# Kernel tuning notes

Hardware: AMD Instinct MI355X
Metric: run time of the kernel (lower is better)

Reference implementation:

```python
import jax, jax.numpy as jnp
import numpy as np

ALPHA = 4.0  # surrogate.Sigmoid(alpha=4.0)
V_TH = 0.1
V_RESET = 0.0

@jax.custom_vjp
def spike(x):
    # Heaviside forward (spikingjelly surrogate.Sigmoid forward pass)
    return (x >= 0).astype(x.dtype)

def _spike_fwd(x):
    return spike(x), x

def _spike_bwd(x, g):
    sig = jax.nn.sigmoid(ALPHA * x)
    return (g * ALPHA * sig * (1.0 - sig),)

spike.defvjp(_spike_fwd, _spike_bwd)

def lif_multistep(x_seq, tau):
    # MultiStepPmLIFNode, hard reset, v clamped to [-2, 2]
    tau = jnp.clip(tau, 0.5, 5.0)
    inv_tau = 1.0 / tau
    def step(v, x):
        v = v + inv_tau * (-(v - V_RESET) + x)
        s = spike(v - V_TH)
        v = jnp.clip(v * (1.0 - s) + V_RESET * s, -2.0, 2.0)
        return v, s
    v0 = jnp.zeros_like(x_seq[0])
    _, spikes = jax.lax.scan(step, v0, x_seq)
    return spikes

def time_distributed_conv(x_seq, W, b, pad):
    # x_seq: [T, B, C, H, W]
    T, B, C, H, Wd = x_seq.shape
    x = x_seq.reshape(T * B, C, H, Wd)
    y = jax.lax.conv_general_dilated(
        x, W, window_strides=(1, 1), padding=[(pad, pad), (pad, pad)],
        dimension_numbers=('NCHW', 'OIHW', 'NCHW'))
    y = y + b[None, :, None, None]
    return y.reshape(T, B, W.shape[0], H, Wd)

def setup_inputs() -> dict:
    key = jax.random.key(0)
    ks = jax.random.split(key, 4)
    B, H, Wd = 8, 128, 128
    return {
        'lr_lab': jax.random.normal(ks[0], (B, 3, H, Wd), dtype=jnp.float32),
        'W1': jax.random.normal(ks[1], (64, 3, 3, 3), dtype=jnp.float32) * 0.1,
        'b1': jnp.zeros((64,), dtype=jnp.float32),
        'tau1': jnp.asarray(2.0, dtype=jnp.float32),
        'W2': jax.random.normal(ks[2], (64, 64, 3, 3), dtype=jnp.float32) * 0.05,
        'b2': jnp.zeros((64,), dtype=jnp.float32),
        'tau2': jnp.asarray(2.0, dtype=jnp.float32),
        'Wh': jax.random.normal(ks[3], (3, 64, 1, 1), dtype=jnp.float32) * 0.1,
        'bh': jnp.zeros((3,), dtype=jnp.float32),
        'T': 5,
    }

def reference(lr_lab, W1, b1, tau1, W2, b2, tau2, Wh, bh, T):
    # H=W=128 is already a power of 2, so the reflect-pad branch is a no-op.
    # TemporalEncoder('repeat') -> [T, B, C, H, W]
    lab_seq = jnp.broadcast_to(lr_lab[None], (T,) + lr_lab.shape)
    # init_conv1: Conv2d(3, 64, 3, pad=1) + MultiStepPmLIFNode
    feat = lif_multistep(time_distributed_conv(lab_seq, W1, b1, pad=1), tau1)
    # init_conv2: Conv2d(64, 64, 3, pad=1) + MultiStepPmLIFNode
    feat = lif_multistep(time_distributed_conv(feat, W2, b2, pad=1), tau2)
    # head_conv: Conv2d(64, 3, 1)
    feat_3 = time_distributed_conv(feat, Wh, bh, pad=0)
    return feat_3
```

## Files before the change

kernel.cpp:

```cpp
#include <hip/hip_runtime.h>


#define NB    8
#define HW    128
#define NPIX  (HW*HW)
#define NT    5

__global__ void k_transpose_w2(const float* __restrict__ W2, float* __restrict__ Wt) {
    int i = blockIdx.x * 256 + threadIdx.x;
    if (i >= 9 * 64 * 64) return;
    int oc = i & 63;
    int ic = (i >> 6) & 63;
    int tap = i >> 12;
    Wt[i] = W2[(oc * 64 + ic) * 9 + tap];
}

__global__ __launch_bounds__(256) void k_conv1_lif1(
    const float* __restrict__ lab, const float* __restrict__ W1,
    const float* __restrict__ b1, const float* __restrict__ tau1,
    unsigned long long* __restrict__ smask)
{
#pragma clang fp contract(off)
    __shared__ float w1s[64 * 27];
    __shared__ float b1s[64];
    {
        int tid = threadIdx.x;
        for (int e = tid; e < 64 * 27; e += 256) w1s[e] = W1[e];
        if (tid < 64) b1s[tid] = b1[tid];
        __syncthreads();
    }
    int g = blockIdx.x * 256 + threadIdx.x;
    int oc = g & 63;
    int x = (g >> 6) & (HW - 1);
    int y = (g >> 13) & (HW - 1);
    int b = g >> 20;

    const float* wbase = w1s + oc * 27;
    const float* ibase = lab + b * 3 * NPIX;
    float acc = 0.f;
    for (int kh = 0; kh < 3; ++kh) {
        int yy = y + kh - 1;
        if ((unsigned)yy >= (unsigned)HW) continue;
        for (int kw = 0; kw < 3; ++kw) {
            int xx = x + kw - 1;
            if ((unsigned)xx >= (unsigned)HW) continue;
            const float* px = ibase + yy * HW + xx;
#pragma unroll
            for (int ic = 0; ic < 3; ++ic) {
                acc = __builtin_fmaf(wbase[ic * 9 + kh * 3 + kw], px[ic * NPIX], acc);
            }
        }
    }
    float xin = acc + b1s[oc];

    float tauc = fminf(fmaxf(tau1[0], 0.5f), 5.0f);
    float it = 1.0f / tauc;

    float v = 0.f;
    unsigned bits = 0;
    for (int t = 0; t < NT; ++t) {
        float d = xin - v;
        float m = it * d;
        v = v + m;
        bool s = (v - 0.1f) >= 0.f;
        float vr = s ? 0.f : v;
        vr = fmaxf(vr, -2.f);
        vr = fminf(vr, 2.f);
        v = vr;
        if (s) bits |= (1u << t);
    }
    for (int t = 0; t < NT; ++t) {
        unsigned long long bal = __ballot((bits >> t) & 1);
        if (oc == 0) smask[((size_t)(b * NT + t) * NPIX) + y * HW + x] = bal;
    }
}

#define SEG(IC0, IC1, M, SH, PN)                                        \
    for (int ic = IC0; ic < IC1; ++ic) {                                \
        unsigned wb = wtu[ic * 64];                                     \
        _Pragma("unroll")                                               \
        for (int p = 0; p < 8; ++p) {                                   \
            unsigned sel = wb & (unsigned)(-(int)((M[p] >> (ic - SH)) & 1u)); \
            acc[p][PN] = acc[p][PN] + __uint_as_float(sel);             \
        }                                                               \
    }

#define TAP(KH, KW, SEGS) {                                             \
    const int yy = y + KH - 1;                                          \
    const bool vy = (unsigned)yy < (unsigned)HW;                        \
    unsigned Mlo[8], Mhi[8];                                            \
    _Pragma("unroll")                                                   \
    for (int p = 0; p < 8; ++p) {                                       \
        int xx = x0 + KW - 1 + p;                                       \
        unsigned long long mm = (vy && (unsigned)xx < (unsigned)HW)     \
                                ? smb[yy * HW + xx] : 0ULL;             \
        Mlo[p] = (unsigned)mm; Mhi[p] = (unsigned)(mm >> 32);           \
    }                                                                   \
    const unsigned* wtu = (const unsigned*)(Wt + (KH * 3 + KW) * 4096) + oc; \
    SEGS }

__global__ __launch_bounds__(256) void k_conv2_lif2(
    const unsigned long long* __restrict__ smask,
    const float* __restrict__ Wt, const float* __restrict__ b2,
    const float* __restrict__ tau2, unsigned long long* __restrict__ s2m)
{
#pragma clang fp contract(off)
    const int tid = threadIdx.x;
    const int oc = tid & 63;
    const int wid = __builtin_amdgcn_readfirstlane(blockIdx.x * 4 + (tid >> 6));
    const int b = wid >> 11;
    const int rem = wid & 2047;
    const int y = rem >> 4;
    const int x0 = (rem & 15) * 8;

    const float b2oc = b2[oc];
    float tauc = fminf(fmaxf(tau2[0], 0.5f), 5.0f);
    const float it = 1.0f / tauc;

    float v[8];
    for (int t = 0; t < NT; ++t) {
        float acc[8][4];
#pragma unroll
        for (int p = 0; p < 8; ++p) {
            acc[p][0] = 0.f; acc[p][1] = 0.f; acc[p][2] = 0.f; acc[p][3] = 0.f;
        }
        const unsigned long long* smb = smask + (size_t)(b * NT + t) * NPIX;

        TAP(0, 0, SEG(0,32,Mlo,0,0)  SEG(32,64,Mhi,32,0))
        TAP(0, 1, SEG(0,32,Mlo,0,0)  SEG(32,64,Mhi,32,0))
        TAP(0, 2, SEG(0,24,Mlo,0,0)  SEG(24,32,Mlo,0,1)  SEG(32,64,Mhi,32,1))
        TAP(1, 0, SEG(0,32,Mlo,0,1)  SEG(32,64,Mhi,32,1))
        TAP(1, 1, SEG(0,32,Mlo,0,1)  SEG(32,48,Mhi,32,1) SEG(48,64,Mhi,32,2))
        TAP(1, 2, SEG(0,32,Mlo,0,2)  SEG(32,64,Mhi,32,2))
        TAP(2, 0, SEG(0,32,Mlo,0,2)  SEG(32,64,Mhi,32,2))
        TAP(2, 1, SEG(0,8,Mlo,0,2)   SEG(8,32,Mlo,0,3)   SEG(32,64,Mhi,32,3))
        TAP(2, 2, SEG(0,32,Mlo,0,3)  SEG(32,64,Mhi,32,3))

        unsigned long long* s2mb = s2m + (size_t)(b * NT + t) * NPIX;
#pragma unroll
        for (int p = 0; p < 8; ++p) {
            float x2 = (((acc[p][0] + acc[p][1]) + acc[p][2]) + acc[p][3]) + b2oc;
            float vp = (t == 0) ? 0.f : v[p];
            float d = x2 - vp;
            float m = it * d;
            vp = vp + m;
            bool s = (vp - 0.1f) >= 0.f;
            float vr = s ? 0.f : vp;
            vr = fmaxf(vr, -2.f);
            vr = fminf(vr, 2.f);
            v[p] = vr;
            unsigned long long bal = __ballot(s);
            if (oc == 0) s2mb[y * HW + x0 + p] = bal;
        }
    }
}

__global__ __launch_bounds__(256) void k_head(
    const unsigned long long* __restrict__ s2m, const float* __restrict__ Wh,
    const float* __restrict__ bh, float* __restrict__ out)
{
#pragma clang fp contract(off)
    __shared__ float whs[192];
    __shared__ float bhs[3];
    {
        int tid = threadIdx.x;
        if (tid < 192) whs[tid] = Wh[tid];
        if (tid < 3) bhs[tid] = bh[tid];
        __syncthreads();
    }
    int g = blockIdx.x * 256 + threadIdx.x;
    int px = g & (NPIX - 1);
    int r = g >> 14;
    int b = r & 7;
    int t = r >> 3;

    unsigned long long m = s2m[(size_t)(b * NT + t) * NPIX + px];
    unsigned mlo = (unsigned)m, mhi = (unsigned)(m >> 32);
    float c0 = 0.f, c1 = 0.f, c2 = 0.f;
    for (int oc = 0; oc < 32; ++oc) {
        unsigned bit = (mlo >> oc) & 1u;
        if (bit) { c0 = c0 + whs[oc]; c1 = c1 + whs[64 + oc]; c2 = c2 + whs[128 + oc]; }
    }
    for (int oc = 32; oc < 64; ++oc) {
        unsigned bit = (mhi >> (oc - 32)) & 1u;
        if (bit) { c0 = c0 + whs[oc]; c1 = c1 + whs[64 + oc]; c2 = c2 + whs[128 + oc]; }
    }
    int obase = ((t * NB + b) * 3) * NPIX + px;
    out[obase] = c0 + bhs[0];
    out[obase + NPIX] = c1 + bhs[1];
    out[obase + 2 * NPIX] = c2 + bhs[2];
}

extern "C" void kernel_launch(void* const* d_in, const int* in_sizes, int n_in,
                              void* d_out, int out_size, void* d_ws, size_t ws_size,
                              hipStream_t stream) {
    const float* lab  = (const float*)d_in[0];
    const float* W1   = (const float*)d_in[1];
    const float* b1   = (const float*)d_in[2];
    const float* tau1 = (const float*)d_in[3];
    const float* W2   = (const float*)d_in[4];
    const float* b2   = (const float*)d_in[5];
    const float* tau2 = (const float*)d_in[6];
    const float* Wh   = (const float*)d_in[7];
    const float* bh   = (const float*)d_in[8];
    float* out = (float*)d_out;

    const size_t SZ_SM = (size_t)NB * NT * NPIX * 8;
    const size_t SZ_WT = 9 * 64 * 64 * 4;
    if (ws_size < 2 * SZ_SM + SZ_WT) return;

    char* ws = (char*)d_ws;
    unsigned long long* smask = (unsigned long long*)ws;
    unsigned long long* s2m   = (unsigned long long*)(ws + SZ_SM);
    float* Wt                 = (float*)(ws + 2 * SZ_SM);

    hipLaunchKernelGGL(k_transpose_w2, dim3(144), dim3(256), 0, stream, W2, Wt);
    hipLaunchKernelGGL(k_conv1_lif1, dim3(NB * 64 * NPIX / 256), dim3(256), 0, stream,
                       lab, W1, b1, tau1, smask);
    hipLaunchKernelGGL(k_conv2_lif2, dim3(4096), dim3(256), 0, stream,
                       smask, Wt, b2, tau2, s2m);
    hipLaunchKernelGGL(k_head, dim3(NT * NB * NPIX / 256), dim3(256), 0, stream,
                       s2m, Wh, bh, out);
}
```

Measured before the change: 2.488 ms.

## Remap conv2 so lanes own pixels and waves own output channels

Conv2 now assigns one pixel to each lane and 16 output channels to each wave. Every weight is therefore a wave-uniform scalar load, and bit selection uses a signed bitfield extract. Spikes are stored as one byte per channel instead of a 64-bit ballot mask, and the head kernel reads 64 byte planes. This removes the per-lane weight gathers, but the spike masks are reloaded for every output channel and the intermediate spike buffer grows eightfold.

```diff
diff --git a/kernel.cpp b/kernel.cpp
--- a/kernel.cpp
+++ b/kernel.cpp
@@ -6,13 +6,21 @@
 #define NPIX  (HW*HW)
 #define NT    5
 
-__global__ void k_transpose_w2(const float* __restrict__ W2, float* __restrict__ Wt) {
+__device__ __forceinline__ unsigned negbit(unsigned m, int off) {
+#if defined(__has_builtin) && __has_builtin(__builtin_amdgcn_sbfe)
+    return (unsigned)__builtin_amdgcn_sbfe((int)m, off, 1);
+#else
+    return (unsigned)((int)(m << (31 - off)) >> 31);
+#endif
+}
+
+__global__ void k_transpose_w2(const float* __restrict__ W2, float* __restrict__ Wt2) {
     int i = blockIdx.x * 256 + threadIdx.x;
-    if (i >= 9 * 64 * 64) return;
-    int oc = i & 63;
-    int ic = (i >> 6) & 63;
-    int tap = i >> 12;
-    Wt[i] = W2[(oc * 64 + ic) * 9 + tap];
+    if (i >= 64 * 9 * 64) return;
+    int ic = i & 63;
+    int tap = (i >> 6) % 9;
+    int oc = i / (9 * 64);
+    Wt2[i] = W2[(oc * 64 + ic) * 9 + tap];
 }
 
 __global__ __launch_bounds__(256) void k_conv1_lif1(
@@ -75,88 +83,75 @@
     }
 }
 
-#define SEG(IC0, IC1, M, SH, PN)                                        \
+#define SEGB(TAP, IC0, IC1, PN)                                         \
+    _Pragma("unroll")                                                   \
     for (int ic = IC0; ic < IC1; ++ic) {                                \
-        unsigned wb = wtu[ic * 64];                                     \
-        _Pragma("unroll")                                               \
-        for (int p = 0; p < 8; ++p) {                                   \
-            unsigned sel = wb & (unsigned)(-(int)((M[p] >> (ic - SH)) & 1u)); \
-            acc[p][PN] = acc[p][PN] + __uint_as_float(sel);             \
-        }                                                               \
-    }
-
-#define TAP(KH, KW, SEGS) {                                             \
+        unsigned nb = negbit((ic < 32) ? mlo : mhi, ic & 31);           \
+        unsigned sel = wq[TAP * 64 + ic] & nb;                          \
+        a##PN = a##PN + __uint_as_float(sel);                           \
+    }
+
+#define TAPB(KH, KW, SEGS) {                                            \
     const int yy = y + KH - 1;                                          \
-    const bool vy = (unsigned)yy < (unsigned)HW;                        \
-    unsigned Mlo[8], Mhi[8];                                            \
-    _Pragma("unroll")                                                   \
-    for (int p = 0; p < 8; ++p) {                                       \
-        int xx = x0 + KW - 1 + p;                                       \
-        unsigned long long mm = (vy && (unsigned)xx < (unsigned)HW)     \
-                                ? smb[yy * HW + xx] : 0ULL;             \
-        Mlo[p] = (unsigned)mm; Mhi[p] = (unsigned)(mm >> 32);           \
-    }                                                                   \
-    const unsigned* wtu = (const unsigned*)(Wt + (KH * 3 + KW) * 4096) + oc; \
+    const int xx = x + KW - 1;                                          \
+    unsigned long long mm = 0ULL;                                       \
+    if (((unsigned)yy < (unsigned)HW) && ((unsigned)xx < (unsigned)HW)) \
+        mm = smb[yy * HW + xx];                                         \
+    const unsigned mlo = (unsigned)mm, mhi = (unsigned)(mm >> 32);      \
     SEGS }
 
 __global__ __launch_bounds__(256) void k_conv2_lif2(
     const unsigned long long* __restrict__ smask,
-    const float* __restrict__ Wt, const float* __restrict__ b2,
-    const float* __restrict__ tau2, unsigned long long* __restrict__ s2m)
+    const float* __restrict__ Wt2, const float* __restrict__ b2,
+    const float* __restrict__ tau2, unsigned char* __restrict__ s2b)
 {
 #pragma clang fp contract(off)
     const int tid = threadIdx.x;
-    const int oc = tid & 63;
-    const int wid = __builtin_amdgcn_readfirstlane(blockIdx.x * 4 + (tid >> 6));
-    const int b = wid >> 11;
-    const int rem = wid & 2047;
-    const int y = rem >> 4;
-    const int x0 = (rem & 15) * 8;
-
-    const float b2oc = b2[oc];
+    const int lane = tid & 63;
+    const int wv = __builtin_amdgcn_readfirstlane(tid >> 6);
+    const int pos = blockIdx.x;
+    const int b = pos >> 8;
+    const int rem = pos & 255;
+    const int y = rem >> 1;
+    const int x = (rem & 1) * 64 + lane;
+
     float tauc = fminf(fmaxf(tau2[0], 0.5f), 5.0f);
     const float it = 1.0f / tauc;
 
-    float v[8];
-    for (int t = 0; t < NT; ++t) {
-        float acc[8][4];
-#pragma unroll
-        for (int p = 0; p < 8; ++p) {
-            acc[p][0] = 0.f; acc[p][1] = 0.f; acc[p][2] = 0.f; acc[p][3] = 0.f;
-        }
-        const unsigned long long* smb = smask + (size_t)(b * NT + t) * NPIX;
-
-        TAP(0, 0, SEG(0,32,Mlo,0,0)  SEG(32,64,Mhi,32,0))
-        TAP(0, 1, SEG(0,32,Mlo,0,0)  SEG(32,64,Mhi,32,0))
-        TAP(0, 2, SEG(0,24,Mlo,0,0)  SEG(24,32,Mlo,0,1)  SEG(32,64,Mhi,32,1))
-        TAP(1, 0, SEG(0,32,Mlo,0,1)  SEG(32,64,Mhi,32,1))
-        TAP(1, 1, SEG(0,32,Mlo,0,1)  SEG(32,48,Mhi,32,1) SEG(48,64,Mhi,32,2))
-        TAP(1, 2, SEG(0,32,Mlo,0,2)  SEG(32,64,Mhi,32,2))
-        TAP(2, 0, SEG(0,32,Mlo,0,2)  SEG(32,64,Mhi,32,2))
-        TAP(2, 1, SEG(0,8,Mlo,0,2)   SEG(8,32,Mlo,0,3)   SEG(32,64,Mhi,32,3))
-        TAP(2, 2, SEG(0,32,Mlo,0,3)  SEG(32,64,Mhi,32,3))
-
-        unsigned long long* s2mb = s2m + (size_t)(b * NT + t) * NPIX;
-#pragma unroll
-        for (int p = 0; p < 8; ++p) {
-            float x2 = (((acc[p][0] + acc[p][1]) + acc[p][2]) + acc[p][3]) + b2oc;
-            float vp = (t == 0) ? 0.f : v[p];
-            float d = x2 - vp;
+    for (int ocl = 0; ocl < 16; ++ocl) {
+        const int oc = wv * 16 + ocl;
+        const unsigned* wq = (const unsigned*)(Wt2 + oc * 576);
+        const float b2oc = b2[oc];
+        float v = 0.f;
+        for (int t = 0; t < NT; ++t) {
+            const unsigned long long* smb = smask + (size_t)(b * NT + t) * NPIX;
+            float a0 = 0.f, a1 = 0.f, a2 = 0.f, a3 = 0.f;
+            TAPB(0, 0, SEGB(0, 0, 64, 0))
+            TAPB(0, 1, SEGB(1, 0, 64, 0))
+            TAPB(0, 2, SEGB(2, 0, 24, 0) SEGB(2, 24, 64, 1))
+            TAPB(1, 0, SEGB(3, 0, 64, 1))
+            TAPB(1, 1, SEGB(4, 0, 48, 1) SEGB(4, 48, 64, 2))
+            TAPB(1, 2, SEGB(5, 0, 64, 2))
+            TAPB(2, 0, SEGB(6, 0, 64, 2))
+            TAPB(2, 1, SEGB(7, 0, 8, 2) SEGB(7, 8, 64, 3))
+            TAPB(2, 2, SEGB(8, 0, 64, 3))
+
+            float x2 = (((a0 + a1) + a2) + a3) + b2oc;
+            float d = x2 - v;
             float m = it * d;
-            vp = vp + m;
+            float vp = v + m;
             bool s = (vp - 0.1f) >= 0.f;
             float vr = s ? 0.f : vp;
             vr = fmaxf(vr, -2.f);
             vr = fminf(vr, 2.f);
-            v[p] = vr;
-            unsigned long long bal = __ballot(s);
-            if (oc == 0) s2mb[y * HW + x0 + p] = bal;
+            v = vr;
+            s2b[((size_t)(b * NT + t) * 64 + oc) * NPIX + y * HW + x] = (unsigned char)s;
         }
     }
 }
 
 __global__ __launch_bounds__(256) void k_head(
-    const unsigned long long* __restrict__ s2m, const float* __restrict__ Wh,
+    const unsigned char* __restrict__ s2b, const float* __restrict__ Wh,
     const float* __restrict__ bh, float* __restrict__ out)
 {
 #pragma clang fp contract(off)
@@ -174,16 +169,14 @@
     int b = r & 7;
     int t = r >> 3;
 
-    unsigned long long m = s2m[(size_t)(b * NT + t) * NPIX + px];
-    unsigned mlo = (unsigned)m, mhi = (unsigned)(m >> 32);
+    const unsigned char* sp = s2b + ((size_t)(b * NT + t) * 64) * NPIX + px;
     float c0 = 0.f, c1 = 0.f, c2 = 0.f;
-    for (int oc = 0; oc < 32; ++oc) {
-        unsigned bit = (mlo >> oc) & 1u;
-        if (bit) { c0 = c0 + whs[oc]; c1 = c1 + whs[64 + oc]; c2 = c2 + whs[128 + oc]; }
-    }
-    for (int oc = 32; oc < 64; ++oc) {
-        unsigned bit = (mhi >> (oc - 32)) & 1u;
-        if (bit) { c0 = c0 + whs[oc]; c1 = c1 + whs[64 + oc]; c2 = c2 + whs[128 + oc]; }
+    for (int oc = 0; oc < 64; ++oc) {
+        if (sp[oc * NPIX]) {
+            c0 = c0 + whs[oc];
+            c1 = c1 + whs[64 + oc];
+            c2 = c2 + whs[128 + oc];
+        }
     }
     int obase = ((t * NB + b) * 3) * NPIX + px;
     out[obase] = c0 + bhs[0];
@@ -206,19 +199,20 @@
     float* out = (float*)d_out;
 
     const size_t SZ_SM = (size_t)NB * NT * NPIX * 8;
-    const size_t SZ_WT = 9 * 64 * 64 * 4;
-    if (ws_size < 2 * SZ_SM + SZ_WT) return;
+    const size_t SZ_S2 = (size_t)NB * NT * 64 * NPIX;
+    const size_t SZ_WT = 64 * 9 * 64 * 4;
+    if (ws_size < SZ_SM + SZ_S2 + SZ_WT) return;
 
     char* ws = (char*)d_ws;
     unsigned long long* smask = (unsigned long long*)ws;
-    unsigned long long* s2m   = (unsigned long long*)(ws + SZ_SM);
-    float* Wt                 = (float*)(ws + 2 * SZ_SM);
-
-    hipLaunchKernelGGL(k_transpose_w2, dim3(144), dim3(256), 0, stream, W2, Wt);
+    unsigned char* s2b        = (unsigned char*)(ws + SZ_SM);
+    float* Wt2                = (float*)(ws + SZ_SM + SZ_S2);
+
+    hipLaunchKernelGGL(k_transpose_w2, dim3(144), dim3(256), 0, stream, W2, Wt2);
     hipLaunchKernelGGL(k_conv1_lif1, dim3(NB * 64 * NPIX / 256), dim3(256), 0, stream,
                        lab, W1, b1, tau1, smask);
-    hipLaunchKernelGGL(k_conv2_lif2, dim3(4096), dim3(256), 0, stream,
-                       smask, Wt, b2, tau2, s2m);
+    hipLaunchKernelGGL(k_conv2_lif2, dim3(2048), dim3(256), 0, stream,
+                       smask, Wt2, b2, tau2, s2b);
     hipLaunchKernelGGL(k_head, dim3(NT * NB * NPIX / 256), dim3(256), 0, stream,
-                       s2m, Wh, bh, out);
-}
+                       s2b, Wh, bh, out);
+}
```

New measurement: 2.888 ms. 16.1% more time.
